# Optimization experiments

Hardware: AMD Instinct MI355X
Metric: run time of the kernel (lower is better)

Reference implementation:

```python
import jax, jax.numpy as jnp
import numpy as np

B, S, HID = 2, 2048, 2048
NH, NKV, D = 32, 8, 64
M = 256          # FAVOR+ random features
CHUNK = 128      # causal chunk size
EPS = 1e-6


def setup_inputs():
    key = jax.random.key(0)
    ks = jax.random.split(key, 7)
    hidden_states = jax.random.normal(ks[0], (B, S, HID), jnp.float32)
    # RoPE tables (HF Llama style): [B, S, D]
    inv_freq = 1.0 / (10000.0 ** (jnp.arange(0, D, 2, dtype=jnp.float32) / D))
    freqs = jnp.arange(S, dtype=jnp.float32)[:, None] * inv_freq[None, :]   # [S, D/2]
    emb = jnp.concatenate([freqs, freqs], axis=-1)                          # [S, D]
    cos = jnp.broadcast_to(jnp.cos(emb)[None], (B, S, D)).astype(jnp.float32)
    sin = jnp.broadcast_to(jnp.sin(emb)[None], (B, S, D)).astype(jnp.float32)
    sc = 0.02
    Wq = jax.random.normal(ks[1], (NH * D, HID), jnp.float32) * sc
    Wk = jax.random.normal(ks[2], (NKV * D, HID), jnp.float32) * sc
    Wv = jax.random.normal(ks[3], (NKV * D, HID), jnp.float32) * sc
    Wo = jax.random.normal(ks[4], (HID, NH * D), jnp.float32) * sc
    proj = jax.random.normal(ks[5], (M, D), jnp.float32)  # FAVOR+ random projection
    return {"hidden_states": hidden_states, "cos": cos, "sin": sin,
            "Wq": Wq, "Wk": Wk, "Wv": Wv, "Wo": Wo, "proj": proj}


def rotate_half(x):
    x1, x2 = x[..., : x.shape[-1] // 2], x[..., x.shape[-1] // 2:]
    return jnp.concatenate([-x2, x1], axis=-1)


def favor_features(x, proj, is_query):
    # FAVOR+ positive softmax-kernel features: phi(x) = exp(Wx' - |x'|^2/2 - stab)/sqrt(m)
    dn = x.shape[-1] ** -0.25
    xn = x * dn                                            # data normalizer d^{-1/4}
    xp = jnp.einsum('bhsd,md->bhsm', xn, proj)             # [B,H,S,M]
    sq = 0.5 * jnp.sum(xn * xn, axis=-1, keepdims=True)
    if is_query:
        stab = jnp.max(xp, axis=-1, keepdims=True)
    else:
        stab = jnp.max(xp, axis=(-1, -2), keepdims=True)
    return (jnp.exp(xp - sq - stab) + EPS) / jnp.sqrt(jnp.asarray(M, xp.dtype))


def causal_linear_attention(phi_q, phi_k, v):
    # phi_q/phi_k: [B,H,S,M], v: [B,H,S,D]; causal chunked prefix formulation
    Bh, H, T, m = phi_q.shape
    d = v.shape[-1]
    nc = T // CHUNK
    qc = phi_q.reshape(Bh, H, nc, CHUNK, m)
    kc = phi_k.reshape(Bh, H, nc, CHUNK, m)
    vc = v.reshape(Bh, H, nc, CHUNK, d)
    # per-chunk KV state and key sums
    kv = jnp.einsum('bhscm,bhscd->bhsmd', kc, vc)          # [B,H,nc,M,D]
    kz = jnp.sum(kc, axis=3)                               # [B,H,nc,M]
    kv_pre = jnp.cumsum(kv, axis=2) - kv                   # exclusive prefix
    kz_pre = jnp.cumsum(kz, axis=2) - kz
    inter = jnp.einsum('bhscm,bhsmd->bhscd', qc, kv_pre)
    inter_z = jnp.einsum('bhscm,bhsm->bhsc', qc, kz_pre)
    # intra-chunk causal part
    mask = jnp.tril(jnp.ones((CHUNK, CHUNK), phi_q.dtype))
    scores = jnp.einsum('bhscm,bhstm->bhsct', qc, kc) * mask
    intra = jnp.einsum('bhsct,bhstd->bhscd', scores, vc)
    intra_z = jnp.sum(scores, axis=-1)
    out = (inter + intra) / (inter_z + intra_z + EPS)[..., None]
    return out.reshape(Bh, H, T, d)


def reference(hidden_states, cos, sin, Wq, Wk, Wv, Wo, proj):
    b, s, _ = hidden_states.shape
    q = (hidden_states @ Wq.T).reshape(b, s, NH, D).transpose(0, 2, 1, 3)   # [B,NH,S,D]
    k = (hidden_states @ Wk.T).reshape(b, s, NKV, D).transpose(0, 2, 1, 3)  # [B,NKV,S,D]
    v = (hidden_states @ Wv.T).reshape(b, s, NKV, D).transpose(0, 2, 1, 3)
    c, si = cos[:, None, :, :], sin[:, None, :, :]
    q = q * c + rotate_half(q) * si
    k = k * c + rotate_half(k) * si
    groups = NH // NKV
    k = jnp.repeat(k, groups, axis=1)
    v = jnp.repeat(v, groups, axis=1)
    phi_q = favor_features(q, proj, is_query=True)
    phi_k = favor_features(k, proj, is_query=False)
    attn = causal_linear_attention(phi_q, phi_k, v)                         # [B,NH,S,D]
    attn = attn.transpose(0, 2, 1, 3).reshape(b, s, NH * D)
    return attn @ Wo.T
```

## Files before the change

### kernel.cpp

```cpp
#include <hip/hip_runtime.h>
#include <hip/hip_bf16.h>

#define SEQ   2048
#define NHEAD 32
#define NKVH  8
#define DH    64
#define MFEAT 256
#define NCH   16
#define EPSF  1e-6f

typedef __hip_bfloat16 bf16;
typedef unsigned short u16;
typedef __attribute__((ext_vector_type(8))) short short8;
typedef __attribute__((ext_vector_type(4))) float f32x4;

__device__ __forceinline__ float b2f(bf16 x){ return __bfloat162float(x); }
__device__ __forceinline__ bf16  f2b(float x){ return __float2bfloat16(x); }
__device__ __forceinline__ u16   f2u(float x){ bf16 h = __float2bfloat16(x); return *reinterpret_cast<u16*>(&h); }

__device__ __forceinline__ bool probe_f32(const unsigned* __restrict__ p){
  return (p[0] & 0xFFFFu) == 0u;
}
__device__ __forceinline__ float loadIn(const void* __restrict__ ptr, size_t idx, bool f32){
  return f32 ? ((const float*)ptr)[idx] : b2f(((const bf16*)ptr)[idx]);
}

__device__ __forceinline__ void cp16(u16* lds, const u16* g){
  __builtin_amdgcn_global_load_lds((const __attribute__((address_space(1))) unsigned*)g,
      (__attribute__((address_space(3))) unsigned*)lds, 16, 0, 0);
}

#define MFMA16(a,b,c) __builtin_amdgcn_mfma_f32_16x16x32_bf16(a,b,c,0,0,0)

__global__ __launch_bounds__(256) void conv_kernel(const void* __restrict__ src,
    u16* __restrict__ dst, const unsigned* __restrict__ probe)
{
  const bool f32in = probe_f32(probe);
  size_t i = ((size_t)blockIdx.x*256 + threadIdx.x)*4;
  #pragma unroll
  for (int j=0;j<4;++j) dst[i+j] = f2u(loadIn(src, i+j, f32in));
}

__global__ __launch_bounds__(256) void gemm_mfma(const u16* __restrict__ A,
    const u16* __restrict__ W, float* __restrict__ oq, float* __restrict__ ok,
    float* __restrict__ ov, void* __restrict__ outAny, int K, int N, int mode,
    const void* __restrict__ cosg, const void* __restrict__ sing,
    const unsigned* __restrict__ probe)
{
  __shared__ __align__(16) u16 sA[4096];
  __shared__ __align__(16) u16 sB[4096];
  const int tid = threadIdx.x;
  const int lane = tid & 63, wave = tid >> 6;
  const int c0 = blockIdx.x*128, r0 = blockIdx.y*128;
  const int wm = wave & 1, wn = wave >> 1;
  f32x4 acc[4][4] = {};

  const int ch0 = wave*64 + lane, ch1 = 256 + wave*64 + lane;
  const u16* gA0 = A + (size_t)(r0 + (ch0>>2))*K + (ch0&3)*8;
  const u16* gA1 = A + (size_t)(r0 + (ch1>>2))*K + (ch1&3)*8;
  const u16* gB0 = W + (size_t)(c0 + (ch0>>2))*K + (ch0&3)*8;
  const u16* gB1 = W + (size_t)(c0 + (ch1>>2))*K + (ch1&3)*8;
  u16* lA0 = &sA[(wave*64)*8];  u16* lA1 = &sA[(256 + wave*64)*8];
  u16* lB0 = &sB[(wave*64)*8];  u16* lB1 = &sB[(256 + wave*64)*8];

  const u16* pA = &sA[(wm*64 + (lane&15))*32 + (lane>>4)*8];
  const u16* pB = &sB[(wn*64 + (lane&15))*32 + (lane>>4)*8];

  for (int k0 = 0; k0 < K; k0 += 32) {
    cp16(lA0, gA0 + k0); cp16(lA1, gA1 + k0);
    cp16(lB0, gB0 + k0); cp16(lB1, gB1 + k0);
    __syncthreads();
    short8 af[4], bfv[4];
    #pragma unroll
    for (int mt=0;mt<4;++mt) af[mt]  = *(const short8*)(pA + mt*512);
    #pragma unroll
    for (int nt=0;nt<4;++nt) bfv[nt] = *(const short8*)(pB + nt*512);
    #pragma unroll
    for (int mt=0;mt<4;++mt)
      #pragma unroll
      for (int nt=0;nt<4;++nt)
        acc[mt][nt] = MFMA16(af[mt], bfv[nt], acc[mt][nt]);
    __syncthreads();
  }

  const int rbase = r0 + wm*64 + (lane>>4)*4;
  const int cbase = c0 + wn*64 + (lane&15);
  if (mode == 0) {
    const bool f32o = probe_f32(probe);
    #pragma unroll
    for (int mt=0;mt<4;++mt)
      #pragma unroll
      for (int nt=0;nt<4;++nt)
        #pragma unroll
        for (int rg=0;rg<4;++rg){
          int r = rbase + mt*16 + rg, c = cbase + nt*16;
          float v = acc[mt][nt][rg];
          if (f32o) ((float*)outAny)[(size_t)r*N + c] = v;
          else      ((u16*)outAny)[(size_t)r*N + c] = f2u(v);
        }
  } else {
    const bool f32in = probe_f32(probe);
    const float dn = 0.3535533905932738f;
    #pragma unroll
    for (int nt=0;nt<4;++nt){
      int cc = cbase + nt*16;
      float* dst; int H2, cl; bool isv = false;
      if (cc < 2048){ dst = oq; H2 = 32; cl = cc; }
      else if (cc < 2560){ dst = ok; H2 = 8; cl = cc - 2048; }
      else { dst = ov; H2 = 8; cl = cc - 2560; isv = true; }
      int hh = cl>>6, dd = cl&63;
      float sgn = (dd < 32) ? -1.f : 1.f;
      #pragma unroll
      for (int mt=0;mt<4;++mt)
        #pragma unroll
        for (int rg=0;rg<4;++rg){
          int r = rbase + mt*16 + rg;
          int bb = r>>11, s = r&2047;
          float v = acc[mt][nt][rg];
          if (!isv){
            float vp = acc[mt][nt^2][rg];
            size_t ci = ((size_t)bb*SEQ + s)*DH + dd;
            float cv = loadIn(cosg, ci, f32in);
            float sv = loadIn(sing, ci, f32in);
            v = (v*cv + sgn*vp*sv) * dn;
          }
          dst[(((size_t)bb*H2 + hh)*SEQ + s)*DH + dd] = v;
        }
    }
  }
}

__global__ __launch_bounds__(256) void phi_mfma(const float* __restrict__ xn,
    const u16* __restrict__ projb, float* __restrict__ rmaxk,
    const float* __restrict__ stabk, u16* __restrict__ phi, int mode)
{
  __shared__ __align__(16) u16 sA[64*80];
  __shared__ __align__(16) u16 sP[256*80];
  __shared__ float sq[64];
  const int tid = threadIdx.x, lane = tid & 63, wave = tid >> 6;
  const size_t row0 = (size_t)blockIdx.x * 64;

  #pragma unroll
  for (int l = 0; l < 8; ++l){
    int v8 = tid + l*256;
    int off = v8*8; int m = off>>6, d = off&63;
    *(short8*)&sP[m*80 + d] = ((const short8*)projb)[v8];
  }
  {
    int r = tid >> 2, qq = tid & 3;
    const float* src = xn + (row0 + r)*DH + qq*16;
    float s = 0.f;
    u16 tmp[16];
    #pragma unroll
    for (int i=0;i<16;i+=4){
      float4 v4 = *(const float4*)&src[i];
      s += v4.x*v4.x + v4.y*v4.y + v4.z*v4.z + v4.w*v4.w;
      tmp[i] = f2u(v4.x); tmp[i+1] = f2u(v4.y); tmp[i+2] = f2u(v4.z); tmp[i+3] = f2u(v4.w);
    }
    *(short8*)&sA[r*80 + qq*16]     = *(short8*)&tmp[0];
    *(short8*)&sA[r*80 + qq*16 + 8] = *(short8*)&tmp[8];
    s += __shfl_xor(s, 1, 64);
    s += __shfl_xor(s, 2, 64);
    if (qq == 0) sq[r] = 0.5f*s;
  }
  __syncthreads();

  f32x4 acc[16] = {};
  const u16* pA = &sA[(wave*16 + (lane&15))*80 + (lane>>4)*8];
  short8 af0 = *(const short8*)(pA);
  short8 af1 = *(const short8*)(pA + 32);
  #pragma unroll
  for (int nt=0; nt<16; ++nt){
    const u16* pB = &sP[(nt*16 + (lane&15))*80 + (lane>>4)*8];
    short8 b0 = *(const short8*)(pB);
    short8 b1 = *(const short8*)(pB + 32);
    acc[nt] = MFMA16(af0, b0, acc[nt]);
    acc[nt] = MFMA16(af1, b1, acc[nt]);
  }

  float mx[4];
  #pragma unroll
  for (int rg=0; rg<4; ++rg){
    float m = acc[0][rg];
    #pragma unroll
    for (int nt=1; nt<16; ++nt) m = fmaxf(m, acc[nt][rg]);
    m = fmaxf(m, __shfl_xor(m, 1, 64));
    m = fmaxf(m, __shfl_xor(m, 2, 64));
    m = fmaxf(m, __shfl_xor(m, 4, 64));
    m = fmaxf(m, __shfl_xor(m, 8, 64));
    mx[rg] = m;
  }
  const int rloc = wave*16 + (lane>>4)*4;
  if (mode == 1){
    if ((lane & 15) == 0){
      #pragma unroll
      for (int rg=0;rg<4;++rg) rmaxk[row0 + rloc + rg] = mx[rg];
    }
    return;
  }
  float stab[4];
  if (mode == 0){
    #pragma unroll
    for (int rg=0;rg<4;++rg) stab[rg] = mx[rg];
  } else {
    float s = stabk[row0 >> 11];
    #pragma unroll
    for (int rg=0;rg<4;++rg) stab[rg] = s;
  }
  float sqr[4];
  #pragma unroll
  for (int rg=0;rg<4;++rg) sqr[rg] = sq[rloc + rg];
  #pragma unroll
  for (int nt=0;nt<16;++nt){
    #pragma unroll
    for (int rg=0;rg<4;++rg){
      float val = (__expf(fminf(acc[nt][rg] - sqr[rg] - stab[rg], 0.f)) + EPSF) * 0.0625f;
      phi[(row0 + rloc + rg)*MFEAT + nt*16 + (lane&15)] = f2u(val);
    }
  }
}

__global__ void stab_reduce_kernel(const float* __restrict__ rmaxk, float* __restrict__ stabk){
  __shared__ float red[256];
  int bk = blockIdx.x;
  float mx = -1e30f;
  for (int i = threadIdx.x; i < SEQ; i += 256) mx = fmaxf(mx, rmaxk[(size_t)bk*SEQ + i]);
  red[threadIdx.x] = mx; __syncthreads();
  for (int off=128; off>0; off>>=1){
    if ((int)threadIdx.x < off) red[threadIdx.x] = fmaxf(red[threadIdx.x], red[threadIdx.x+off]);
    __syncthreads();
  }
  if (threadIdx.x==0) stabk[bk] = red[0];
}

__global__ __launch_bounds__(256) void kvchunk_kernel(const bf16* __restrict__ phik,
    const float* __restrict__ vbuf, float* __restrict__ kv, float* __restrict__ kz)
{
  int blk = blockIdx.x; int bk = blk >> 4, c = blk & 15;
  const bf16* Kc = phik + ((size_t)bk*SEQ + c*128)*MFEAT;
  const float* Vc = vbuf + ((size_t)bk*SEQ + c*128)*DH;
  __shared__ float sV[128*64];
  for (int l=0;l<32;++l){ int idx = threadIdx.x + l*256; sV[idx] = Vc[idx]; }
  __syncthreads();
  int m = threadIdx.x;
  float acc[64] = {}; float az = 0.f;
  for (int t=0;t<128;++t){
    float ph = b2f(Kc[(size_t)t*MFEAT + m]);
    az += ph;
    const float4* vr = (const float4*)&sV[t*64];
    #pragma unroll
    for (int d4=0; d4<16; ++d4){
      float4 v4 = vr[d4];
      acc[d4*4+0] += ph*v4.x; acc[d4*4+1] += ph*v4.y;
      acc[d4*4+2] += ph*v4.z; acc[d4*4+3] += ph*v4.w;
    }
  }
  float* out = kv + (size_t)blk*MFEAT*DH + (size_t)m*DH;
  #pragma unroll
  for (int d4=0; d4<16; ++d4)
    ((float4*)out)[d4] = make_float4(acc[d4*4],acc[d4*4+1],acc[d4*4+2],acc[d4*4+3]);
  kz[(size_t)blk*MFEAT + m] = az;
}

__global__ void scan_kernel(float* __restrict__ p, int inner, int nc, int total){
  int t = blockIdx.x*256 + threadIdx.x;
  if (t >= total) return;
  int outer = t / inner, rem = t - outer*inner;
  float* base = p + (size_t)outer*nc*inner + rem;
  float run = 0.f;
  for (int c=0;c<nc;++c){
    float v = base[(size_t)c*inner];
    base[(size_t)c*inner] = run;
    run += v;
  }
}

__global__ __launch_bounds__(256) void attn_mfma(
    const u16* __restrict__ phiq, const u16* __restrict__ phik,
    const float* __restrict__ vbuf, const float* __restrict__ kvp,
    const float* __restrict__ kzp, u16* __restrict__ attnout)
{
  __shared__ __align__(16) u16 smem[28288];
  __shared__ float sZ[128];
  const int tid = threadIdx.x, lane = tid & 63, wave = tid >> 6;
  const int blk = blockIdx.x;
  const int c = blk & 15, h = (blk >> 4) & 31, b = blk >> 9;
  const int kvh = h >> 2;
  const u16* Q   = phiq + (((size_t)(b*NHEAD+h)*SEQ) + c*128)*MFEAT;
  const u16* Kc  = phik + (((size_t)(b*NKVH+kvh)*SEQ) + c*128)*MFEAT;
  const float* Vc  = vbuf + (((size_t)(b*NKVH+kvh)*SEQ) + c*128)*DH;
  const float* KVp = kvp + ((size_t)((b*NKVH+kvh)*NCH + c))*MFEAT*DH;
  const float* KZp = kzp + ((size_t)((b*NKVH+kvh)*NCH + c))*MFEAT;

  u16* sQ   = smem;
  u16* sK   = smem + 4096;
  u16* sKVT = smem + 8192;
  u16* sP   = smem;
  u16* sVT  = smem + 17408;

  f32x4 accS[2][8] = {};
  f32x4 accO[2][5] = {};

  const int ch0 = wave*64 + lane, ch1 = 256 + wave*64 + lane;
  const u16* gQ0 = Q  + (ch0>>2)*MFEAT + (ch0&3)*8;
  const u16* gQ1 = Q  + (ch1>>2)*MFEAT + (ch1&3)*8;
  const u16* gK0 = Kc + (ch0>>2)*MFEAT + (ch0&3)*8;
  const u16* gK1 = Kc + (ch1>>2)*MFEAT + (ch1&3)*8;
  u16* lQ0 = &sQ[(wave*64)*8];  u16* lQ1 = &sQ[(256+wave*64)*8];
  u16* lK0 = &sK[(wave*64)*8];  u16* lK1 = &sK[(256+wave*64)*8];

  for (int k0 = 0; k0 < MFEAT; k0 += 32) {
    cp16(lQ0, gQ0 + k0); cp16(lQ1, gQ1 + k0);
    cp16(lK0, gK0 + k0); cp16(lK1, gK1 + k0);
    #pragma unroll
    for (int i=0;i<8;++i){
      int idx = tid + i*256;
      int m = idx >> 6, d = idx & 63;
      sKVT[d*72 + m] = f2u(KVp[(size_t)(k0+m)*DH + d]);
    }
    if (tid < 32) sKVT[64*72 + tid] = f2u(KZp[k0 + tid]);
    __syncthreads();
    short8 af0, af1;
    const u16* pQ = &sQ[(wave*32 + (lane&15))*32 + (lane>>4)*8];
    af0 = *(const short8*)(pQ);
    af1 = *(const short8*)(pQ + 512);
    #pragma unroll
    for (int nt=0;nt<8;++nt){
      short8 bk = *(const short8*)&sK[(nt*16 + (lane&15))*32 + (lane>>4)*8];
      accS[0][nt] = MFMA16(af0, bk, accS[0][nt]);
      accS[1][nt] = MFMA16(af1, bk, accS[1][nt]);
    }
    #pragma unroll
    for (int nt=0;nt<5;++nt){
      short8 bi = *(const short8*)&sKVT[(nt*16 + (lane&15))*72 + (lane>>4)*8];
      accO[0][nt] = MFMA16(af0, bi, accO[0][nt]);
      accO[1][nt] = MFMA16(af1, bi, accO[1][nt]);
    }
    __syncthreads();
  }

  #pragma unroll
  for (int mt=0;mt<2;++mt){
    int rowb = wave*32 + mt*16 + (lane>>4)*4;
    #pragma unroll
    for (int nt=0;nt<8;++nt){
      int col = nt*16 + (lane&15);
      #pragma unroll
      for (int rg=0;rg<4;++rg){
        int row = rowb + rg;
        float v = (col <= row) ? accS[mt][nt][rg] : 0.f;
        sP[row*136 + col] = f2u(v);
      }
    }
  }
  #pragma unroll
  for (int i=0;i<32;++i){
    int idx = tid + i*256;
    int t = idx >> 6, d = idx & 63;
    sVT[d*136 + t] = f2u(Vc[idx]);
  }
  if (tid < 128) sVT[64*136 + tid] = 0x3F80;
  __syncthreads();

  #pragma unroll
  for (int kc=0;kc<4;++kc){
    const u16* pP = &sP[(wave*32 + (lane&15))*136 + kc*32 + (lane>>4)*8];
    short8 pa0 = *(const short8*)(pP);
    short8 pa1 = *(const short8*)(pP + 16*136);
    #pragma unroll
    for (int nt=0;nt<5;++nt){
      short8 bv = *(const short8*)&sVT[(nt*16 + (lane&15))*136 + kc*32 + (lane>>4)*8];
      accO[0][nt] = MFMA16(pa0, bv, accO[0][nt]);
      accO[1][nt] = MFMA16(pa1, bv, accO[1][nt]);
    }
  }

  if ((lane & 15) == 0){
    #pragma unroll
    for (int mt=0;mt<2;++mt){
      int rowb = wave*32 + mt*16 + (lane>>4)*4;
      #pragma unroll
      for (int rg=0;rg<4;++rg) sZ[rowb + rg] = accO[mt][4][rg];
    }
  }
  __syncthreads();
  const int d0 = lane & 15;
  #pragma unroll
  for (int mt=0;mt<2;++mt){
    int rowb = wave*32 + mt*16 + (lane>>4)*4;
    #pragma unroll
    for (int rg=0;rg<4;++rg){
      int row = rowb + rg;
      float inv = 1.0f / (sZ[row] + EPSF);
      int sg = c*128 + row;
      size_t ob = (((size_t)b*SEQ + sg)*NHEAD + h)*DH;
      #pragma unroll
      for (int nt=0;nt<4;++nt)
        attnout[ob + nt*16 + d0] = f2u(accO[mt][nt][rg] * inv);
    }
  }
}

extern "C" void kernel_launch(void* const* d_in, const int* in_sizes, int n_in,
                              void* d_out, int out_size, void* d_ws, size_t ws_size,
                              hipStream_t stream)
{
  const void* hidden = d_in[0];
  const void* cosg   = d_in[1];
  const void* sing   = d_in[2];
  const void* Wq     = d_in[3];
  const void* Wk     = d_in[4];
  const void* Wv     = d_in[5];
  const void* Wo     = d_in[6];
  const void* proj   = d_in[7];
  const unsigned* probe = (const unsigned*)d_in[1];

  float* ws = (float*)d_ws;
  float* xnq   = ws;
  float* kv    = ws;
  float* kz    = ws + 4194304;
  float* rmaxk = ws + 4259840;
  float* stabk = ws + 4292608;
  float* xnk   = ws + 8388608;
  float* vbuf  = ws + 10485760;
  u16*   projb = (u16*) (ws + 12582912);
  bf16*  phiq  = (bf16*)(ws + 12591104);
  bf16*  phik  = (bf16*)(ws + 29368320);
  u16*   hb    = (u16*) (ws + 33562624);
  u16*   attn  = (u16*) (ws + 33562624);
  u16*   wqkv  = (u16*) (ws + 37756928);
  u16*   wob   = (u16*) (ws + 37756928);

  conv_kernel<<<8192, 256, 0, stream>>>(hidden, hb, probe);
  conv_kernel<<<4096, 256, 0, stream>>>(Wq, wqkv,           probe);
  conv_kernel<<<1024, 256, 0, stream>>>(Wk, wqkv + 4194304, probe);
  conv_kernel<<<1024, 256, 0, stream>>>(Wv, wqkv + 5242880, probe);
  conv_kernel<<<16,   256, 0, stream>>>(proj, projb, probe);

  gemm_mfma<<<dim3(24,32), 256, 0, stream>>>(hb, wqkv, xnq, xnk, vbuf, nullptr,
                                             2048, 3072, 1, cosg, sing, probe);
  conv_kernel<<<4096, 256, 0, stream>>>(Wo, wob, probe);

  phi_mfma<<<2048, 256, 0, stream>>>(xnq, projb, nullptr, nullptr, (u16*)phiq, 0);
  phi_mfma<<<512,  256, 0, stream>>>(xnk, projb, rmaxk, nullptr, nullptr, 1);
  stab_reduce_kernel<<<16, 256, 0, stream>>>(rmaxk, stabk);
  phi_mfma<<<512,  256, 0, stream>>>(xnk, projb, nullptr, stabk, (u16*)phik, 2);

  kvchunk_kernel<<<256, 256, 0, stream>>>(phik, vbuf, kv, kz);
  scan_kernel<<<1024, 256, 0, stream>>>(kv, MFEAT*DH, NCH, 16*MFEAT*DH);
  scan_kernel<<<16,   256, 0, stream>>>(kz, MFEAT,    NCH, 16*MFEAT);

  attn_mfma<<<1024, 256, 0, stream>>>((const u16*)phiq, (const u16*)phik,
                                      vbuf, kv, kz, attn);

  gemm_mfma<<<dim3(16,32), 256, 0, stream>>>(attn, wob, nullptr, nullptr, nullptr,
                                             d_out, 2048, 2048, 0, nullptr, nullptr, probe);
}
```

Measured before the change: 499.0 us.

## Double GEMM K-tile to 64 and XOR-swizzle shared-memory layout

The MFMA GEMM now stages a 64-wide K slice per iteration instead of 32, halving the number of barrier pairs and loop iterations. Shared tiles are stored with an XOR swizzle of the 16-byte chunk index by row, so the MFMA fragment reads avoid LDS bank conflicts. Shared memory per block doubles to 32 KB, which may lower occupancy, and there is still no double-buffering.

```diff
diff --git a/kernel.cpp b/kernel.cpp
--- a/kernel.cpp
+++ b/kernel.cpp
@@ -47,39 +47,50 @@
     const void* __restrict__ cosg, const void* __restrict__ sing,
     const unsigned* __restrict__ probe)
 {
-  __shared__ __align__(16) u16 sA[4096];
-  __shared__ __align__(16) u16 sB[4096];
+  __shared__ __align__(16) u16 sA[8192];
+  __shared__ __align__(16) u16 sB[8192];
   const int tid = threadIdx.x;
   const int lane = tid & 63, wave = tid >> 6;
   const int c0 = blockIdx.x*128, r0 = blockIdx.y*128;
   const int wm = wave & 1, wn = wave >> 1;
   f32x4 acc[4][4] = {};
 
-  const int ch0 = wave*64 + lane, ch1 = 256 + wave*64 + lane;
-  const u16* gA0 = A + (size_t)(r0 + (ch0>>2))*K + (ch0&3)*8;
-  const u16* gA1 = A + (size_t)(r0 + (ch1>>2))*K + (ch1&3)*8;
-  const u16* gB0 = W + (size_t)(c0 + (ch0>>2))*K + (ch0&3)*8;
-  const u16* gB1 = W + (size_t)(c0 + (ch1>>2))*K + (ch1&3)*8;
-  u16* lA0 = &sA[(wave*64)*8];  u16* lA1 = &sA[(256 + wave*64)*8];
-  u16* lB0 = &sB[(wave*64)*8];  u16* lB1 = &sB[(256 + wave*64)*8];
-
-  const u16* pA = &sA[(wm*64 + (lane&15))*32 + (lane>>4)*8];
-  const u16* pB = &sB[(wn*64 + (lane&15))*32 + (lane>>4)*8];
-
-  for (int k0 = 0; k0 < K; k0 += 32) {
-    cp16(lA0, gA0 + k0); cp16(lA1, gA1 + k0);
-    cp16(lB0, gB0 + k0); cp16(lB1, gB1 + k0);
+  const u16* gA[4]; const u16* gB[4];
+  u16* lA[4]; u16* lB[4];
+  #pragma unroll
+  for (int i=0;i<4;++i){
+    int idx = wave*64 + lane + i*256;
+    int row = idx >> 3, c8 = (idx & 7) ^ (row & 7);
+    gA[i] = A + (size_t)(r0+row)*K + c8*8;
+    gB[i] = W + (size_t)(c0+row)*K + c8*8;
+    lA[i] = &sA[(wave*64 + i*256)*8];
+    lB[i] = &sB[(wave*64 + i*256)*8];
+  }
+  const int q = lane >> 4, l15 = lane & 15;
+
+  for (int k0 = 0; k0 < K; k0 += 64) {
+    #pragma unroll
+    for (int i=0;i<4;++i){ cp16(lA[i], gA[i]+k0); cp16(lB[i], gB[i]+k0); }
     __syncthreads();
-    short8 af[4], bfv[4];
-    #pragma unroll
-    for (int mt=0;mt<4;++mt) af[mt]  = *(const short8*)(pA + mt*512);
-    #pragma unroll
-    for (int nt=0;nt<4;++nt) bfv[nt] = *(const short8*)(pB + nt*512);
-    #pragma unroll
-    for (int mt=0;mt<4;++mt)
-      #pragma unroll
-      for (int nt=0;nt<4;++nt)
-        acc[mt][nt] = MFMA16(af[mt], bfv[nt], acc[mt][nt]);
+    #pragma unroll
+    for (int ks=0; ks<2; ++ks){
+      short8 af[4], bfv[4];
+      #pragma unroll
+      for (int mt=0;mt<4;++mt){
+        int mrow = wm*64 + mt*16 + l15;
+        af[mt] = *(const short8*)&sA[mrow*64 + ((ks*4+q)^(mrow&7))*8];
+      }
+      #pragma unroll
+      for (int nt=0;nt<4;++nt){
+        int nrow = wn*64 + nt*16 + l15;
+        bfv[nt] = *(const short8*)&sB[nrow*64 + ((ks*4+q)^(nrow&7))*8];
+      }
+      #pragma unroll
+      for (int mt=0;mt<4;++mt)
+        #pragma unroll
+        for (int nt=0;nt<4;++nt)
+          acc[mt][nt] = MFMA16(af[mt], bfv[nt], acc[mt][nt]);
+    }
     __syncthreads();
   }
 
```

New measurement: 547.5 us. +9.7%, slower.
